# Kernel tuning notes

Measured on AMD Instinct MI355X. Metric: run time of the kernel, lower is better.

The kernel has to match this reference:

```python
import jax, jax.numpy as jnp
import numpy as np


def setup_inputs() -> dict:
    key = jax.random.key(0)
    k1, = jax.random.split(key, 1)
    B, H, W, C = 16, 64, 64, 256
    x = jax.random.normal(k1, (B, H, W, C), dtype=jnp.float32)
    gamma = jnp.zeros((1,), dtype=jnp.float32)
    return {"x": x, "gamma": gamma}


def reference(x, gamma):
    B, H, W, C = x.shape
    a = x.reshape(B, H * W, C)                      # [B, HW, C]
    # aTa[b, i, j] = sum_n a[b, n, i] * a[b, n, j]  -> [B, C, C]
    aTa = jnp.einsum('bni,bnj->bij', a, a)
    attn = jax.nn.softmax(aTa, axis=-1)             # softmax over last channel axis
    # aaTa[b, n, j] = sum_i a[b, n, i] * attn[b, i, j]
    aaTa = jnp.einsum('bni,bij->bnj', a, attn)      # [B, HW, C]
    aaTa = aaTa.reshape(B, H, W, C)
    return gamma * aaTa + x
```

## Files before the change

### kernel.cpp

```cpp
#include <hip/hip_runtime.h>
#include <hip/hip_bf16.h>


#define BB 16
#define NN 4096
#define CC 256
#define SPLITK 8
#define KCHUNK (NN / SPLITK)

typedef __attribute__((ext_vector_type(4))) short short4v;
typedef __attribute__((ext_vector_type(8))) short short8v;
typedef __attribute__((ext_vector_type(4))) float floatx4;

__device__ __forceinline__ unsigned short f2bf(float f) {
    unsigned int u = __float_as_uint(f);
    u += 0x7fffu + ((u >> 16) & 1u);
    return (unsigned short)(u >> 16);
}
__device__ __forceinline__ short4v cvt4(floatx4 v) {
    short4v r;
    r[0] = (short)f2bf(v[0]); r[1] = (short)f2bf(v[1]);
    r[2] = (short)f2bf(v[2]); r[3] = (short)f2bf(v[3]);
    return r;
}

__global__ __launch_bounds__(256) void k_transpose(const float* __restrict__ x,
                                                   unsigned short* __restrict__ aT) {
    __shared__ unsigned short tile[64 * 68];
    const int b  = blockIdx.z;
    const int n0 = blockIdx.x * 64;
    const int c0 = blockIdx.y * 64;
    const int t  = threadIdx.x;
    const int q4 = (t & 15) * 4;
    const int tr = t >> 4;

    const float* xb = x + ((size_t)b * NN + n0) * CC + c0;
    for (int r = 0; r < 4; ++r) {
        int row = tr + 16 * r;
        floatx4 v = *(const floatx4*)(xb + (size_t)row * CC + q4);
        *(short4v*)&tile[row * 68 + q4] = cvt4(v);
    }
    __syncthreads();
    unsigned short* aTb = aT + ((size_t)b * CC + c0) * NN + n0;
    for (int r = 0; r < 4; ++r) {
        int c = tr + 16 * r;
        short4v v;
        v[0] = (short)tile[(q4 + 0) * 68 + c];
        v[1] = (short)tile[(q4 + 1) * 68 + c];
        v[2] = (short)tile[(q4 + 2) * 68 + c];
        v[3] = (short)tile[(q4 + 3) * 68 + c];
        *(short4v*)(aTb + (size_t)c * NN + q4) = v;
    }
}

__global__ __launch_bounds__(256) void k_gemm1(const unsigned short* __restrict__ aT,
                                               float* __restrict__ part) {
    __shared__ unsigned short Ap[64 * 72];
    __shared__ unsigned short Bp[256 * 72];
    const int i0    = blockIdx.x * 64;
    const int b     = blockIdx.y;
    const int split = blockIdx.z;
    const int t  = threadIdx.x;
    const int w  = t >> 6, l = t & 63;
    const int lk = (l >> 4) * 8;
    const int lm = l & 15;
    const int sc = t >> 4;
    const int sk = (t & 15) * 4;

    const unsigned short* Abase = aT + ((size_t)b * CC + i0) * NN;
    const unsigned short* Bbase = aT + (size_t)b * CC * NN;

    floatx4 acc[4][4] = {};
    const int kbeg = split * KCHUNK;
    for (int k0 = kbeg; k0 < kbeg + KCHUNK; k0 += 64) {
        #pragma unroll
        for (int r = 0; r < 4; ++r) {
            int i = sc + 16 * r;
            *(short4v*)&Ap[i * 72 + sk] = *(const short4v*)(Abase + (size_t)i * NN + k0 + sk);
        }
        #pragma unroll
        for (int r = 0; r < 16; ++r) {
            int j = sc + 16 * r;
            *(short4v*)&Bp[j * 72 + sk] = *(const short4v*)(Bbase + (size_t)j * NN + k0 + sk);
        }
        __syncthreads();
        #pragma unroll
        for (int ks = 0; ks < 64; ks += 32) {
            short8v af[4], bf[4];
            #pragma unroll
            for (int mt = 0; mt < 4; ++mt)
                af[mt] = *(const short8v*)&Ap[(mt * 16 + lm) * 72 + ks + lk];
            #pragma unroll
            for (int nt = 0; nt < 4; ++nt)
                bf[nt] = *(const short8v*)&Bp[(w * 64 + nt * 16 + lm) * 72 + ks + lk];
            #pragma unroll
            for (int mt = 0; mt < 4; ++mt)
                #pragma unroll
                for (int nt = 0; nt < 4; ++nt)
                    acc[mt][nt] = __builtin_amdgcn_mfma_f32_16x16x32_bf16(af[mt], bf[nt], acc[mt][nt], 0, 0, 0);
        }
        __syncthreads();
    }
    const int orow = (l >> 4) * 4;
    float* pout = part + ((size_t)(split * BB + b) * CC) * CC;
    #pragma unroll
    for (int mt = 0; mt < 4; ++mt)
        #pragma unroll
        for (int nt = 0; nt < 4; ++nt)
            #pragma unroll
            for (int r = 0; r < 4; ++r) {
                int i = i0 + mt * 16 + orow + r;
                int j = w * 64 + nt * 16 + lm;
                pout[(size_t)i * CC + j] = acc[mt][nt][r];
            }
}

__global__ __launch_bounds__(256) void k_softmax(const float* __restrict__ part,
                                                 unsigned short* __restrict__ attnT) {
    const int w = threadIdx.x >> 6;
    const int l = threadIdx.x & 63;
    const int row = blockIdx.x * 4 + w;
    const int b = row >> 8;
    const int i = row & 255;
    float v0 = 0.f, v1 = 0.f, v2 = 0.f, v3 = 0.f;
    #pragma unroll
    for (int s = 0; s < SPLITK; ++s) {
        const float* p = part + ((size_t)(s * BB + b) * CC + i) * CC;
        v0 += p[l]; v1 += p[l + 64]; v2 += p[l + 128]; v3 += p[l + 192];
    }
    float m = fmaxf(fmaxf(v0, v1), fmaxf(v2, v3));
    for (int off = 32; off >= 1; off >>= 1) m = fmaxf(m, __shfl_xor(m, off, 64));
    v0 = __expf(v0 - m); v1 = __expf(v1 - m); v2 = __expf(v2 - m); v3 = __expf(v3 - m);
    float s = v0 + v1 + v2 + v3;
    for (int off = 32; off >= 1; off >>= 1) s += __shfl_xor(s, off, 64);
    float rs = 1.0f / s;
    unsigned short* o = attnT + (size_t)b * CC * CC + i;
    o[(size_t)(l +   0) * CC] = f2bf(v0 * rs);
    o[(size_t)(l +  64) * CC] = f2bf(v1 * rs);
    o[(size_t)(l + 128) * CC] = f2bf(v2 * rs);
    o[(size_t)(l + 192) * CC] = f2bf(v3 * rs);
}

__global__ __launch_bounds__(256) void k_gemm2(const float* __restrict__ x,
                                               const unsigned short* __restrict__ attnT,
                                               const float* __restrict__ gamma,
                                               float* __restrict__ out) {
    __shared__ unsigned short At[64 * 72];
    __shared__ unsigned short Bt[256 * 72];
    const int n0 = blockIdx.x * 64;
    const int b  = blockIdx.y;
    const int t  = threadIdx.x;
    const int w  = t >> 6, l = t & 63;
    const int lk = (l >> 4) * 8, lm = l & 15;
    const int sc = t >> 4, sk = (t & 15) * 4;

    const float*          Abase = x + ((size_t)b * NN + n0) * CC;
    const unsigned short* Bbase = attnT + (size_t)b * CC * CC;

    floatx4 acc[4][4] = {};
    for (int k0 = 0; k0 < CC; k0 += 64) {
        #pragma unroll
        for (int r = 0; r < 4; ++r) {
            int n = sc + 16 * r;
            floatx4 av = *(const floatx4*)(Abase + (size_t)n * CC + k0 + sk);
            *(short4v*)&At[n * 72 + sk] = cvt4(av);
        }
        #pragma unroll
        for (int r = 0; r < 16; ++r) {
            int j = sc + 16 * r;
            *(short4v*)&Bt[j * 72 + sk] = *(const short4v*)(Bbase + (size_t)j * CC + k0 + sk);
        }
        __syncthreads();
        #pragma unroll
        for (int ks = 0; ks < 64; ks += 32) {
            short8v af[4], bf[4];
            #pragma unroll
            for (int mt = 0; mt < 4; ++mt)
                af[mt] = *(const short8v*)&At[(mt * 16 + lm) * 72 + ks + lk];
            #pragma unroll
            for (int nt = 0; nt < 4; ++nt)
                bf[nt] = *(const short8v*)&Bt[(w * 64 + nt * 16 + lm) * 72 + ks + lk];
            #pragma unroll
            for (int mt = 0; mt < 4; ++mt)
                #pragma unroll
                for (int nt = 0; nt < 4; ++nt)
                    acc[mt][nt] = __builtin_amdgcn_mfma_f32_16x16x32_bf16(af[mt], bf[nt], acc[mt][nt], 0, 0, 0);
        }
        __syncthreads();
    }
    const float g = gamma[0];
    const int orow = (l >> 4) * 4;
    #pragma unroll
    for (int mt = 0; mt < 4; ++mt)
        #pragma unroll
        for (int nt = 0; nt < 4; ++nt)
            #pragma unroll
            for (int r = 0; r < 4; ++r) {
                int nr = n0 + mt * 16 + orow + r;
                int j  = w * 64 + nt * 16 + lm;
                size_t idx = ((size_t)b * NN + nr) * CC + j;
                out[idx] = g * acc[mt][nt][r] + x[idx];
            }
}

extern "C" void kernel_launch(void* const* d_in, const int* in_sizes, int n_in,
                              void* d_out, int out_size, void* d_ws, size_t ws_size,
                              hipStream_t stream) {
    const float* x     = (const float*)d_in[0];
    const float* gamma = (const float*)d_in[1];
    float* out = (float*)d_out;

    char* ws = (char*)d_ws;
    unsigned short* aT    = (unsigned short*)ws;
    float*          part  = (float*)(ws + (size_t)BB * CC * NN * 2);
    unsigned short* attnT = (unsigned short*)(ws + (size_t)BB * CC * NN * 2
                                                 + (size_t)SPLITK * BB * CC * CC * 4);

    k_transpose<<<dim3(NN / 64, CC / 64, BB), 256, 0, stream>>>(x, aT);
    k_gemm1   <<<dim3(CC / 64, BB, SPLITK),   256, 0, stream>>>(aT, part);
    k_softmax <<<dim3(BB * CC / 4),           256, 0, stream>>>(part, attnT);
    k_gemm2   <<<dim3(NN / 64, BB),           256, 0, stream>>>(x, attnT, gamma, out);
}
```

Baseline: 179.5 us.

## Fuse transpose into Gram GEMM, reading x directly with a swizzled LDS tile

```diff
diff --git a/kernel.cpp b/kernel.cpp
--- a/kernel.cpp
+++ b/kernel.cpp
@@ -24,93 +24,81 @@
     return r;
 }
 
-__global__ __launch_bounds__(256) void k_transpose(const float* __restrict__ x,
-                                                   unsigned short* __restrict__ aT) {
-    __shared__ unsigned short tile[64 * 68];
-    const int b  = blockIdx.z;
-    const int n0 = blockIdx.x * 64;
-    const int c0 = blockIdx.y * 64;
-    const int t  = threadIdx.x;
-    const int q4 = (t & 15) * 4;
-    const int tr = t >> 4;
-
-    const float* xb = x + ((size_t)b * NN + n0) * CC + c0;
-    for (int r = 0; r < 4; ++r) {
-        int row = tr + 16 * r;
-        floatx4 v = *(const floatx4*)(xb + (size_t)row * CC + q4);
-        *(short4v*)&tile[row * 68 + q4] = cvt4(v);
-    }
-    __syncthreads();
-    unsigned short* aTb = aT + ((size_t)b * CC + c0) * NN + n0;
-    for (int r = 0; r < 4; ++r) {
-        int c = tr + 16 * r;
-        short4v v;
-        v[0] = (short)tile[(q4 + 0) * 68 + c];
-        v[1] = (short)tile[(q4 + 1) * 68 + c];
-        v[2] = (short)tile[(q4 + 2) * 68 + c];
-        v[3] = (short)tile[(q4 + 3) * 68 + c];
-        *(short4v*)(aTb + (size_t)c * NN + q4) = v;
-    }
-}
-
-__global__ __launch_bounds__(256) void k_gemm1(const unsigned short* __restrict__ aT,
-                                               float* __restrict__ part) {
-    __shared__ unsigned short Ap[64 * 72];
-    __shared__ unsigned short Bp[256 * 72];
-    const int i0    = blockIdx.x * 64;
+__global__ __launch_bounds__(256, 1) void k_gemm1(const float* __restrict__ x,
+                                                  float* __restrict__ part) {
+    __shared__ unsigned short P[256 * 72];
+    const int split = blockIdx.x;
     const int b     = blockIdx.y;
-    const int split = blockIdx.z;
+    const int half  = blockIdx.z;
     const int t  = threadIdx.x;
     const int w  = t >> 6, l = t & 63;
     const int lk = (l >> 4) * 8;
     const int lm = l & 15;
-    const int sc = t >> 4;
-    const int sk = (t & 15) * 4;
-
-    const unsigned short* Abase = aT + ((size_t)b * CC + i0) * NN;
-    const unsigned short* Bbase = aT + (size_t)b * CC * NN;
-
-    floatx4 acc[4][4] = {};
-    const int kbeg = split * KCHUNK;
-    for (int k0 = kbeg; k0 < kbeg + KCHUNK; k0 += 64) {
-        #pragma unroll
-        for (int r = 0; r < 4; ++r) {
-            int i = sc + 16 * r;
-            *(short4v*)&Ap[i * 72 + sk] = *(const short4v*)(Abase + (size_t)i * NN + k0 + sk);
-        }
-        #pragma unroll
-        for (int r = 0; r < 16; ++r) {
-            int j = sc + 16 * r;
-            *(short4v*)&Bp[j * 72 + sk] = *(const short4v*)(Bbase + (size_t)j * NN + k0 + sk);
-        }
-        __syncthreads();
+    const int i0 = half * 128;
+    const int wr = (w >> 1) * 64;
+    const int wc = (w & 1) * 128;
+    const unsigned swz = (unsigned)(l & 7) << 3;
+
+    const float* xb = x + ((size_t)b * NN + (size_t)split * KCHUNK) * CC + 4 * l;
+
+    floatx4 pf[16];
+    #pragma unroll
+    for (int p = 0; p < 16; ++p)
+        pf[p] = *(const floatx4*)(xb + (size_t)(w + 4 * p) * CC);
+
+    floatx4 acc[4][8] = {};
+
+    for (int k0 = 0; k0 < KCHUNK; k0 += 64) {
+        short4v s[16];
+        #pragma unroll
+        for (int p = 0; p < 16; ++p) s[p] = cvt4(pf[p]);
+        #pragma unroll
+        for (int j = 0; j < 4; ++j) {
+            short8v oA, oB;
+            #pragma unroll
+            for (int e = 0; e < 8; ++e) { oA[e] = s[e][j]; oB[e] = s[e + 8][j]; }
+            const unsigned c = (unsigned)(4 * l + j);
+            *(short8v*)&P[c * 72 + (((unsigned)(16 * w))     ^ swz)] = oA;
+            *(short8v*)&P[c * 72 + (((unsigned)(16 * w + 8)) ^ swz)] = oB;
+        }
+        __syncthreads();
+        if (k0 + 64 < KCHUNK) {
+            const float* xn = xb + (size_t)(k0 + 64) * CC;
+            #pragma unroll
+            for (int p = 0; p < 16; ++p)
+                pf[p] = *(const floatx4*)(xn + (size_t)(w + 4 * p) * CC);
+        }
         #pragma unroll
         for (int ks = 0; ks < 64; ks += 32) {
-            short8v af[4], bf[4];
-            #pragma unroll
-            for (int mt = 0; mt < 4; ++mt)
-                af[mt] = *(const short8v*)&Ap[(mt * 16 + lm) * 72 + ks + lk];
-            #pragma unroll
-            for (int nt = 0; nt < 4; ++nt)
-                bf[nt] = *(const short8v*)&Bp[(w * 64 + nt * 16 + lm) * 72 + ks + lk];
+            short8v af[4], bf[8];
+            #pragma unroll
+            for (int mt = 0; mt < 4; ++mt) {
+                const unsigned row = (unsigned)(i0 + wr + mt * 16 + lm);
+                af[mt] = *(const short8v*)&P[row * 72 + (((unsigned)(ks + lk)) ^ (((row >> 2) & 7u) << 3))];
+            }
+            #pragma unroll
+            for (int nt = 0; nt < 8; ++nt) {
+                const unsigned row = (unsigned)(wc + nt * 16 + lm);
+                bf[nt] = *(const short8v*)&P[row * 72 + (((unsigned)(ks + lk)) ^ (((row >> 2) & 7u) << 3))];
+            }
             #pragma unroll
             for (int mt = 0; mt < 4; ++mt)
                 #pragma unroll
-                for (int nt = 0; nt < 4; ++nt)
+                for (int nt = 0; nt < 8; ++nt)
                     acc[mt][nt] = __builtin_amdgcn_mfma_f32_16x16x32_bf16(af[mt], bf[nt], acc[mt][nt], 0, 0, 0);
         }
         __syncthreads();
     }
     const int orow = (l >> 4) * 4;
-    float* pout = part + ((size_t)(split * BB + b) * CC) * CC;
+    float* pout = part + (size_t)(split * BB + b) * CC * CC;
     #pragma unroll
     for (int mt = 0; mt < 4; ++mt)
         #pragma unroll
-        for (int nt = 0; nt < 4; ++nt)
+        for (int nt = 0; nt < 8; ++nt)
             #pragma unroll
             for (int r = 0; r < 4; ++r) {
-                int i = i0 + mt * 16 + orow + r;
-                int j = w * 64 + nt * 16 + lm;
+                int i = i0 + wr + mt * 16 + orow + r;
+                int j = wc + nt * 16 + lm;
                 pout[(size_t)i * CC + j] = acc[mt][nt][r];
             }
 }
@@ -211,13 +199,10 @@
     float* out = (float*)d_out;
 
     char* ws = (char*)d_ws;
-    unsigned short* aT    = (unsigned short*)ws;
-    float*          part  = (float*)(ws + (size_t)BB * CC * NN * 2);
-    unsigned short* attnT = (unsigned short*)(ws + (size_t)BB * CC * NN * 2
-                                                 + (size_t)SPLITK * BB * CC * CC * 4);
-
-    k_transpose<<<dim3(NN / 64, CC / 64, BB), 256, 0, stream>>>(x, aT);
-    k_gemm1   <<<dim3(CC / 64, BB, SPLITK),   256, 0, stream>>>(aT, part);
-    k_softmax <<<dim3(BB * CC / 4),           256, 0, stream>>>(part, attnT);
-    k_gemm2   <<<dim3(NN / 64, BB),           256, 0, stream>>>(x, attnT, gamma, out);
-}
+    float*          part  = (float*)ws;
+    unsigned short* attnT = (unsigned short*)(ws + (size_t)SPLITK * BB * CC * CC * 4);
+
+    k_gemm1  <<<dim3(SPLITK, BB, 2),  256, 0, stream>>>(x, part);
+    k_softmax<<<dim3(BB * CC / 4),    256, 0, stream>>>(part, attnT);
+    k_gemm2  <<<dim3(NN / 64, BB),    256, 0, stream>>>(x, attnT, gamma, out);
+}
```

Result: faster. 162.4 us (-9.5%).
